# Optimization experiments

Hardware: AMD Instinct MI355X
Metric: run time of the kernel (lower is better)

Reference implementation:

```python
import jax, jax.numpy as jnp
import numpy as np

HIDDEN = 2048
N_HEADS = 32
N_KV_HEADS = 4
HEAD_DIM = 128
EPS = 1e-6
ROPE_THETA = 1000000.0
B, S = 1, 2048


def setup_inputs() -> dict:
    key = jax.random.key(0)
    ks = jax.random.split(key, 7)
    scale = 0.02
    return {
        "hidden_states": jax.random.normal(ks[0], (B, S, HIDDEN), jnp.float32),
        "wq": jax.random.normal(ks[1], (HIDDEN, N_HEADS * HEAD_DIM), jnp.float32) * scale,
        "wk": jax.random.normal(ks[2], (HIDDEN, N_KV_HEADS * HEAD_DIM), jnp.float32) * scale,
        "wv": jax.random.normal(ks[3], (HIDDEN, N_KV_HEADS * HEAD_DIM), jnp.float32) * scale,
        "wo": jax.random.normal(ks[4], (N_HEADS * HEAD_DIM, HIDDEN), jnp.float32) * scale,
        "q_norm_w": jnp.ones((HEAD_DIM,), jnp.float32),
        "k_norm_w": jnp.ones((HEAD_DIM,), jnp.float32),
    }


def _rmsnorm(x, w, eps=EPS):
    # RMSNorm over last (head_dim) axis, as in Qwen3MoeRMSNorm applied per-head
    var = jnp.mean(jnp.square(x), axis=-1, keepdims=True)
    return x * jax.lax.rsqrt(var + eps) * w


def _rope_cos_sin(seq_len, dtype):
    inv_freq = 1.0 / (ROPE_THETA ** (jnp.arange(0, HEAD_DIM, 2, dtype=jnp.float32) / HEAD_DIM))
    pos = jnp.arange(seq_len, dtype=jnp.float32)
    freqs = pos[:, None] * inv_freq[None, :]          # [S, dh/2]
    emb = jnp.concatenate([freqs, freqs], axis=-1)    # [S, dh]
    return jnp.cos(emb).astype(dtype), jnp.sin(emb).astype(dtype)


def _rotate_half(x):
    h = x.shape[-1] // 2
    return jnp.concatenate([-x[..., h:], x[..., :h]], axis=-1)


def reference(hidden_states, wq, wk, wv, wo, q_norm_w, k_norm_w):
    b, s, _ = hidden_states.shape
    # QKV projections (bias-free)
    q = (hidden_states @ wq).reshape(b, s, N_HEADS, HEAD_DIM)
    k = (hidden_states @ wk).reshape(b, s, N_KV_HEADS, HEAD_DIM)
    v = (hidden_states @ wv).reshape(b, s, N_KV_HEADS, HEAD_DIM)
    # per-head RMSNorm on Q and K
    q = _rmsnorm(q, q_norm_w)
    k = _rmsnorm(k, k_norm_w)
    # RoPE (prefill, start_pos = 0)
    cos, sin = _rope_cos_sin(s, q.dtype)              # [S, dh]
    cos = cos[None, :, None, :]
    sin = sin[None, :, None, :]
    q = q * cos + _rotate_half(q) * sin
    k = k * cos + _rotate_half(k) * sin
    # GQA: repeat KV heads to match Q heads
    groups = N_HEADS // N_KV_HEADS
    k = jnp.repeat(k, groups, axis=2)                 # [B,S,nH,dh]
    v = jnp.repeat(v, groups, axis=2)
    # causal SDPA
    scaling = HEAD_DIM ** -0.5
    scores = jnp.einsum("bqhd,bkhd->bhqk", q, k) * scaling
    causal = jnp.tril(jnp.ones((s, s), dtype=bool))
    scores = jnp.where(causal[None, None], scores, jnp.finfo(scores.dtype).min)
    probs = jax.nn.softmax(scores, axis=-1)
    attn = jnp.einsum("bhqk,bkhd->bqhd", probs, v)    # [B,S,nH,dh]
    attn = attn.reshape(b, s, N_HEADS * HEAD_DIM)
    return attn @ wo
```

## Files before the change

kernel.cpp:

```cpp
#include <hip/hip_runtime.h>
#include <stdint.h>

typedef unsigned short u16;
typedef __bf16 bf16x8 __attribute__((ext_vector_type(8)));
typedef float f32x4 __attribute__((ext_vector_type(4)));

#define SEQ 2048
#define QKV_N 5120
#define QN 4096

#if __has_builtin(__builtin_amdgcn_exp2f)
#define EXP2F __builtin_amdgcn_exp2f
#else
#define EXP2F exp2f
#endif

#define QSC (0.08838834764831845f * 1.4426950408889634f)
#define MLOG2E 17.312340490667560f

#define WAIT_VM(n) asm volatile("s_waitcnt vmcnt(" #n ")" ::: "memory")
#define WAIT_LGKM asm volatile("s_waitcnt lgkmcnt(0)" ::: "memory")
#define FENCE asm volatile("" ::: "memory")
#define BARRIER_RAW do { FENCE; __builtin_amdgcn_s_barrier(); FENCE; } while (0)

__device__ __forceinline__ u16 f2bf(float f) {
  union { float f; unsigned u; } v; v.f = f;
  unsigned r = v.u + 0x7fffu + ((v.u >> 16) & 1u);
  return (u16)(r >> 16);
}
__device__ __forceinline__ u16 f2bf_fast(float f) {
  union { float f; unsigned u; } v; v.f = f;
  return (u16)((v.u + 0x8000u) >> 16);
}
__device__ __forceinline__ float bf2f(u16 b) {
  union { unsigned u; float f; } v; v.u = ((unsigned)b) << 16;
  return v.f;
}

__device__ __forceinline__ void gl2lds16(const void* g, void* l) {
  __builtin_amdgcn_global_load_lds((const __attribute__((address_space(1))) void*)g,
                                   (__attribute__((address_space(3))) void*)l, 16, 0, 0);
}

__global__ __launch_bounds__(256) void k_prep(const float* __restrict__ hidden,
                                              const float* __restrict__ wq, const float* __restrict__ wk,
                                              const float* __restrict__ wv, const float* __restrict__ wo,
                                              u16* __restrict__ hid_bf, u16* __restrict__ WT,
                                              u16* __restrict__ woT) {
  __shared__ float t[32][33];
  int bx = blockIdx.x;
  if (bx < 4096) {
    int i = (bx * 256 + threadIdx.x) * 4;
    float4 v = *(const float4*)(hidden + i);
    ushort4 o;
    o.x = f2bf(v.x); o.y = f2bf(v.y); o.z = f2bf(v.z); o.w = f2bf(v.w);
    *(ushort4*)(hid_bf + i) = o;
    return;
  }
  const float* src; u16* dst; int R, C, cx, cy;
  if (bx < 4096 + 8192) {
    int local = bx - 4096; src = wq; dst = WT; R = 2048; C = 4096;
    cx = local & 127; cy = local >> 7;
  } else if (bx < 4096 + 8192 + 1024) {
    int local = bx - (4096 + 8192); src = wk; dst = WT + (size_t)4096 * 2048; R = 2048; C = 512;
    cx = local & 15; cy = local >> 4;
  } else if (bx < 4096 + 8192 + 2048) {
    int local = bx - (4096 + 8192 + 1024); src = wv; dst = WT + (size_t)4608 * 2048; R = 2048; C = 512;
    cx = local & 15; cy = local >> 4;
  } else {
    int local = bx - (4096 + 8192 + 2048); src = wo; dst = woT; R = 4096; C = 2048;
    cx = local & 63; cy = local >> 6;
  }
  int c0 = cx * 32, r0 = cy * 32;
  int j = threadIdx.x & 31, i0 = threadIdx.x >> 5;
#pragma unroll
  for (int p = 0; p < 4; ++p) {
    int r = i0 + p * 8;
    t[r][j] = src[(size_t)(r0 + r) * C + c0 + j];
  }
  __syncthreads();
#pragma unroll
  for (int p = 0; p < 4; ++p) {
    int r = i0 + p * 8;
    dst[(size_t)(c0 + r) * R + r0 + j] = f2bf(t[j][r]);
  }
}

__global__ __launch_bounds__(256) void k_gemm160(const u16* __restrict__ A, const u16* __restrict__ BT,
                                                 u16* __restrict__ C, int M, int N, int K) {
  __shared__ u16 As[2][128 * 64];
  __shared__ u16 Bs[2][160 * 64];
  const int tid = threadIdx.x;
  const int w = tid >> 6, lane = tid & 63, quad = lane >> 4, l15 = lane & 15;
  const int m0 = blockIdx.y * 128, n0 = blockIdx.x * 160;
  const int mw = (w & 1) * 64, nw = (w >> 1) * 80;

  f32x4 acc[4][5];
#pragma unroll
  for (int i = 0; i < 4; ++i)
#pragma unroll
    for (int j = 0; j < 5; ++j) acc[i][j] = {0.f, 0.f, 0.f, 0.f};

  auto stage = [&](int kt, int buf) {
    const int k0 = kt << 6;
#pragma unroll
    for (int p = 0; p < 4; ++p) {
      int ci = (w * 4 + p) * 64 + lane;
      int row = ci >> 3, gc = (ci & 7) ^ (row & 7);
      gl2lds16(A + (size_t)(m0 + row) * K + k0 + gc * 8, &As[buf][(w * 4 + p) * 512]);
    }
#pragma unroll
    for (int p = 0; p < 5; ++p) {
      int ci = (w * 5 + p) * 64 + lane;
      int row = ci >> 3, gc = (ci & 7) ^ (row & 7);
      gl2lds16(BT + (size_t)(n0 + row) * K + k0 + gc * 8, &Bs[buf][(w * 5 + p) * 512]);
    }
  };

  const int nk = K >> 6;
  stage(0, 0);
  for (int kt = 0; kt < nk; ++kt) {
    WAIT_LGKM;
    BARRIER_RAW;
    if (kt + 1 < nk) {
      stage(kt + 1, (kt + 1) & 1);
      WAIT_VM(9);
    } else {
      WAIT_VM(0);
    }
    BARRIER_RAW;
    const u16* Ac = As[kt & 1];
    const u16* Bc = Bs[kt & 1];
#pragma unroll
    for (int kk = 0; kk < 2; ++kk) {
      bf16x8 a[4], b[5];
#pragma unroll
      for (int mt = 0; mt < 4; ++mt) {
        int row = mw + mt * 16 + l15;
        a[mt] = *(const bf16x8*)(Ac + row * 64 + (((kk * 4 + quad) ^ (row & 7)) * 8));
      }
#pragma unroll
      for (int nt = 0; nt < 5; ++nt) {
        int row = nw + nt * 16 + l15;
        b[nt] = *(const bf16x8*)(Bc + row * 64 + (((kk * 4 + quad) ^ (row & 7)) * 8));
      }
#pragma unroll
      for (int mt = 0; mt < 4; ++mt)
#pragma unroll
        for (int nt = 0; nt < 5; ++nt)
          acc[mt][nt] = __builtin_amdgcn_mfma_f32_16x16x32_bf16(a[mt], b[nt], acc[mt][nt], 0, 0, 0);
    }
  }
#pragma unroll
  for (int mt = 0; mt < 4; ++mt)
#pragma unroll
    for (int nt = 0; nt < 5; ++nt)
#pragma unroll
      for (int r = 0; r < 4; ++r) {
        int row = m0 + mw + mt * 16 + quad * 4 + r;
        int col = n0 + nw + nt * 16 + l15;
        C[(size_t)row * N + col] = f2bf(acc[mt][nt][r]);
      }
}

__global__ __launch_bounds__(256) void k_gemm_sk(const u16* __restrict__ A, const u16* __restrict__ BT,
                                                 float* __restrict__ C, int M, int N, int K) {
  __shared__ u16 As[2][128 * 64];
  __shared__ u16 Bs[2][128 * 64];
  const int tid = threadIdx.x;
  const int w = tid >> 6, lane = tid & 63, quad = lane >> 4, l15 = lane & 15;
  const int m0 = blockIdx.y * 128, n0 = blockIdx.x * 128;
  const int mw = (w & 1) * 64, nw = (w >> 1) * 64;
  const int khalf = K >> 1;
  const int kbase = blockIdx.z * khalf;

  f32x4 acc[4][4];
#pragma unroll
  for (int i = 0; i < 4; ++i)
#pragma unroll
    for (int j = 0; j < 4; ++j) acc[i][j] = {0.f, 0.f, 0.f, 0.f};

  auto stage = [&](int kt, int buf) {
    const int k0 = kbase + (kt << 6);
#pragma unroll
    for (int p = 0; p < 4; ++p) {
      int ci = (w * 4 + p) * 64 + lane;
      int row = ci >> 3, gc = (ci & 7) ^ (row & 7);
      gl2lds16(A + (size_t)(m0 + row) * K + k0 + gc * 8, &As[buf][(w * 4 + p) * 512]);
      gl2lds16(BT + (size_t)(n0 + row) * K + k0 + gc * 8, &Bs[buf][(w * 4 + p) * 512]);
    }
  };

  const int nk = khalf >> 6;
  stage(0, 0);
  for (int kt = 0; kt < nk; ++kt) {
    WAIT_LGKM;
    BARRIER_RAW;
    if (kt + 1 < nk) {
      stage(kt + 1, (kt + 1) & 1);
      WAIT_VM(8);
    } else {
      WAIT_VM(0);
    }
    BARRIER_RAW;
    const u16* Ac = As[kt & 1];
    const u16* Bc = Bs[kt & 1];
#pragma unroll
    for (int kk = 0; kk < 2; ++kk) {
      bf16x8 a[4], b[4];
#pragma unroll
      for (int mt = 0; mt < 4; ++mt) {
        int row = mw + mt * 16 + l15;
        a[mt] = *(const bf16x8*)(Ac + row * 64 + (((kk * 4 + quad) ^ (row & 7)) * 8));
      }
#pragma unroll
      for (int nt = 0; nt < 4; ++nt) {
        int row = nw + nt * 16 + l15;
        b[nt] = *(const bf16x8*)(Bc + row * 64 + (((kk * 4 + quad) ^ (row & 7)) * 8));
      }
#pragma unroll
      for (int mt = 0; mt < 4; ++mt)
#pragma unroll
        for (int nt = 0; nt < 4; ++nt)
          acc[mt][nt] = __builtin_amdgcn_mfma_f32_16x16x32_bf16(a[mt], b[nt], acc[mt][nt], 0, 0, 0);
    }
  }
#pragma unroll
  for (int mt = 0; mt < 4; ++mt)
#pragma unroll
    for (int nt = 0; nt < 4; ++nt)
#pragma unroll
      for (int r = 0; r < 4; ++r) {
        int row = m0 + mw + mt * 16 + quad * 4 + r;
        int col = n0 + nw + nt * 16 + l15;
        atomicAdd(&C[(size_t)row * N + col], acc[mt][nt][r]);
      }
}

__global__ __launch_bounds__(256) void k_post(const u16* __restrict__ QKV,
                                              const float* __restrict__ qw, const float* __restrict__ kw,
                                              u16* __restrict__ qb, u16* __restrict__ kb,
                                              u16* __restrict__ vt) {
  __shared__ u16 t[32][34];
  int bx = blockIdx.x;
  if (bx < 2048) {
    int s = bx;
    int w = threadIdx.x >> 6, lane = threadIdx.x & 63;
    const u16* row = QKV + (size_t)s * QKV_N;
    float inv_freq = EXP2F(-(float)lane * (19.931568569324174f / 64.0f));
    float fr = (float)s * inv_freq;
    float sn, cs;
    __sincosf(fr, &sn, &cs);
    float qw0 = qw[lane], qw1 = qw[lane + 64];
    float kw0 = kw[lane], kw1 = kw[lane + 64];
    for (int item = w; item < 36; item += 4) {
      bool isq = item < 32;
      int h = isq ? item : item - 32;
      int base = isq ? h * 128 : 4096 + h * 128;
      float x0 = bf2f(row[base + lane]), x1 = bf2f(row[base + 64 + lane]);
      float ss = x0 * x0 + x1 * x1;
#pragma unroll
      for (int off = 1; off < 64; off <<= 1) ss += __shfl_xor(ss, off);
      float rr = rsqrtf(ss * (1.0f / 128.0f) + 1e-6f);
      float n0 = x0 * rr * (isq ? qw0 : kw0), n1 = x1 * rr * (isq ? qw1 : kw1);
      float y0 = n0 * cs - n1 * sn;
      float y1 = n1 * cs + n0 * sn;
      if (isq) {
        size_t o = (size_t)s * QN + h * 128 + lane;
        qb[o] = f2bf(y0 * QSC);
        qb[o + 64] = f2bf(y1 * QSC);
      } else {
        size_t o = ((size_t)h * SEQ + s) * 128 + lane;
        kb[o] = f2bf(y0);
        kb[o + 64] = f2bf(y1);
      }
    }
    return;
  }
  int local = bx - 2048;
  int s0 = (local & 63) * 32, d0 = ((local >> 6) & 3) * 32, h = local >> 8;
  int j = threadIdx.x & 31, i0 = threadIdx.x >> 5;
#pragma unroll
  for (int p = 0; p < 4; ++p) {
    int r = i0 + p * 8;
    t[r][j] = QKV[(size_t)(s0 + r) * QKV_N + 4608 + h * 128 + d0 + j];
  }
  __syncthreads();
#pragma unroll
  for (int p = 0; p < 4; ++p) {
    int r = i0 + p * 8;
    vt[((size_t)h * 128 + d0 + r) * SEQ + s0 + j] = t[j][r];
  }
}

__global__ __launch_bounds__(256, 2) void k_flash(const u16* __restrict__ qb_, const u16* __restrict__ kb,
                                                  const u16* __restrict__ vt, u16* __restrict__ attn) {
  __shared__ u16 Ks[2][64 * 128];
  __shared__ u16 Vts[2][128 * 64];
  __shared__ u16 Ps[4][2048];
  const int bx = blockIdx.x;
  const int slot = bx & 255, phase = bx >> 8;
  const int head = slot & 31;
  const int qblk = phase ? (slot >> 5) : 15 - (slot >> 5);
  const int kvh = head >> 3;
  const int q0 = qblk * 128;
  const int tid = threadIdx.x, w = tid >> 6, lane = tid & 63, quad = lane >> 4, l15 = lane & 15;
  const int rowlo0 = q0 + w * 32, rowlo1 = rowlo0 + 16;

  bf16x8 qf[2][4];
#pragma unroll
  for (int mt = 0; mt < 2; ++mt) {
    const u16* qrow = qb_ + (size_t)(rowlo0 + mt * 16 + l15) * QN + head * 128;
#pragma unroll
    for (int ks = 0; ks < 4; ++ks) qf[mt][ks] = *(const bf16x8*)(qrow + ks * 32 + quad * 8);
  }
  f32x4 o[2][8];
#pragma unroll
  for (int mt = 0; mt < 2; ++mt)
#pragma unroll
    for (int i = 0; i < 8; ++i) o[mt][i] = {0.f, 0.f, 0.f, 0.f};
  float lr[2][4] = {{0.f, 0.f, 0.f, 0.f}, {0.f, 0.f, 0.f, 0.f}};

  const u16* kbase = kb + (size_t)kvh * SEQ * 128;
  const u16* vbase = vt + (size_t)kvh * 128 * SEQ;
  u16* pw = Ps[w];

  auto stage = [&](int ti, int buf) {
    const int t0 = ti * 64;
#pragma unroll
    for (int p = 0; p < 4; ++p) {
      int ci = (w * 4 + p) * 64 + lane;
      {
        int row = ci >> 4, gc = (ci & 15) ^ (row & 15);
        gl2lds16(kbase + (size_t)(t0 + row) * 128 + gc * 8, &Ks[buf][(w * 4 + p) * 512]);
      }
      {
        int d = ci >> 3, gc = (ci & 7) ^ (d & 7);
        gl2lds16(vbase + (size_t)d * SEQ + t0 + gc * 8, &Vts[buf][(w * 4 + p) * 512]);
      }
    }
  };

  const int nT = 2 * qblk + 2;
  stage(0, 0);
  for (int ti = 0; ti < nT; ++ti) {
    const int t0 = ti * 64;
    WAIT_LGKM;
    BARRIER_RAW;
    if (ti + 1 < nT) {
      stage(ti + 1, (ti + 1) & 1);
      WAIT_VM(8);
    } else {
      WAIT_VM(0);
    }
    BARRIER_RAW;
    const u16* Kc = Ks[ti & 1];
    const u16* Vc = Vts[ti & 1];

    const bool a0 = t0 < rowlo0 + 16;
    const bool a1 = t0 < rowlo1 + 16;
    if (a1) {
      f32x4 sa[2][4];
#pragma unroll
      for (int mt = 0; mt < 2; ++mt)
#pragma unroll
        for (int nt = 0; nt < 4; ++nt) sa[mt][nt] = {0.f, 0.f, 0.f, 0.f};
#pragma unroll
      for (int nt = 0; nt < 4; ++nt) {
        int row = nt * 16 + l15;
#pragma unroll
        for (int ks = 0; ks < 4; ++ks) {
          bf16x8 kf = *(const bf16x8*)(Kc + row * 128 + (((ks * 4 + quad) ^ (row & 15)) * 8));
          if (a0) sa[0][nt] = __builtin_amdgcn_mfma_f32_16x16x32_bf16(qf[0][ks], kf, sa[0][nt], 0, 0, 0);
          sa[1][nt] = __builtin_amdgcn_mfma_f32_16x16x32_bf16(qf[1][ks], kf, sa[1][nt], 0, 0, 0);
        }
      }
#pragma unroll
      for (int mt = 0; mt < 2; ++mt) {
        if (mt == 0 && !a0) continue;
        const int rl = rowlo0 + mt * 16;
        const bool domask = (t0 + 63 > rl);
        u16* pm = pw + mt * 1024;
#pragma unroll
        for (int nt = 0; nt < 4; ++nt)
#pragma unroll
          for (int r = 0; r < 4; ++r) {
            float p = EXP2F(sa[mt][nt][r] - MLOG2E);
            if (domask) {
              int tcol = t0 + nt * 16 + l15;
              int qrow = rl + quad * 4 + r;
              p = (tcol > qrow) ? 0.f : p;
            }
            sa[mt][nt][r] = p;
            pm[(quad * 4 + r) * 64 + ((nt ^ quad) << 4) + l15] = f2bf_fast(p);
          }
#pragma unroll
        for (int r = 0; r < 4; ++r)
          lr[mt][r] += sa[mt][0][r] + sa[mt][1][r] + sa[mt][2][r] + sa[mt][3][r];
      }
      WAIT_LGKM;
#pragma unroll
      for (int ks2 = 0; ks2 < 2; ++ks2) {
        int col = (ks2 * 32 + quad * 8) ^ ((l15 >> 2) << 4);
        bf16x8 pa0, pa1;
        if (a0) pa0 = *(const bf16x8*)(pw + l15 * 64 + col);
        pa1 = *(const bf16x8*)(pw + 1024 + l15 * 64 + col);
#pragma unroll
        for (int nt2 = 0; nt2 < 8; ++nt2) {
          int d = nt2 * 16 + l15;
          bf16x8 vf = *(const bf16x8*)(Vc + d * 64 + (((ks2 * 4 + quad) ^ (d & 7)) * 8));
          if (a0) o[0][nt2] = __builtin_amdgcn_mfma_f32_16x16x32_bf16(pa0, vf, o[0][nt2], 0, 0, 0);
          o[1][nt2] = __builtin_amdgcn_mfma_f32_16x16x32_bf16(pa1, vf, o[1][nt2], 0, 0, 0);
        }
      }
    }
  }
#pragma unroll
  for (int mt = 0; mt < 2; ++mt) {
    float inv[4];
#pragma unroll
    for (int r = 0; r < 4; ++r) {
      float s = lr[mt][r];
      s += __shfl_xor(s, 1);
      s += __shfl_xor(s, 2);
      s += __shfl_xor(s, 4);
      s += __shfl_xor(s, 8);
      inv[r] = 1.0f / s;
    }
#pragma unroll
    for (int nt2 = 0; nt2 < 8; ++nt2)
#pragma unroll
      for (int r = 0; r < 4; ++r) {
        size_t idx = (size_t)(rowlo0 + mt * 16 + quad * 4 + r) * QN + head * 128 + nt2 * 16 + l15;
        attn[idx] = f2bf_fast(o[mt][nt2][r] * inv[r]);
      }
  }
}

extern "C" void kernel_launch(void* const* d_in, const int* in_sizes, int n_in,
                              void* d_out, int out_size, void* d_ws, size_t ws_size,
                              hipStream_t stream) {
  const float* hidden = (const float*)d_in[0];
  const float* wq = (const float*)d_in[1];
  const float* wk = (const float*)d_in[2];
  const float* wv = (const float*)d_in[3];
  const float* wo = (const float*)d_in[4];
  const float* qnw = (const float*)d_in[5];
  const float* knw = (const float*)d_in[6];
  float* out = (float*)d_out;

  char* ws = (char*)d_ws;
  u16* hid_bf = (u16*)(ws);
  u16* WT = (u16*)(ws + 8388608);
  u16* woT = (u16*)(ws + 29360128);
  u16* QKV = (u16*)(ws + 46137344);
  u16* q_bf = (u16*)(ws + 88080384);
  u16* k_bf = (u16*)(ws + 104857600);
  u16* vt = (u16*)(ws + 106954752);
  u16* attn = (u16*)(ws + 109051904);

  hipMemsetAsync(d_out, 0, (size_t)2048 * 2048 * 4, stream);
  k_prep<<<22528, 256, 0, stream>>>(hidden, wq, wk, wv, wo, hid_bf, WT, woT);
  k_gemm160<<<dim3(32, 16), 256, 0, stream>>>(hid_bf, WT, QKV, 2048, 5120, 2048);
  k_post<<<3072, 256, 0, stream>>>(QKV, qnw, knw, q_bf, k_bf, vt);
  k_flash<<<512, 256, 0, stream>>>(q_bf, k_bf, vt, attn);
  k_gemm_sk<<<dim3(16, 16, 2), 256, 0, stream>>>(attn, woT, out, 2048, 2048, 4096);
}
```

Measured before the change: 325.7 us.

## Pair mirrored causal query blocks per workgroup to balance flash attention work

Each workgroup now handles two 64-row query slabs, one early (a) and one mirrored late (31-a), so every block runs a near-equal number of KV tiles. This replaces the earlier scheme of 128-row contiguous query blocks with long-first ordering, which left per-block work uneven. The trade-off is that each wave's two 16-row tiles are far apart, so the early tile sits idle for most KV iterations and its MFMAs are skipped. Grid size and launch code are assumed to stay at 512 blocks.

```diff
diff --git a/kernel.cpp b/kernel.cpp
--- a/kernel.cpp
+++ b/kernel.cpp
@@ -299,18 +299,18 @@
   __shared__ u16 Vts[2][128 * 64];
   __shared__ u16 Ps[4][2048];
   const int bx = blockIdx.x;
-  const int slot = bx & 255, phase = bx >> 8;
-  const int head = slot & 31;
-  const int qblk = phase ? (slot >> 5) : 15 - (slot >> 5);
+  const int head = bx & 31;
+  const int a = bx >> 5;
   const int kvh = head >> 3;
-  const int q0 = qblk * 128;
   const int tid = threadIdx.x, w = tid >> 6, lane = tid & 63, quad = lane >> 4, l15 = lane & 15;
-  const int rowlo0 = q0 + w * 32, rowlo1 = rowlo0 + 16;
+  const int rA = a * 64 + w * 16;
+  const int rB = (31 - a) * 64 + w * 16;
 
   bf16x8 qf[2][4];
 #pragma unroll
   for (int mt = 0; mt < 2; ++mt) {
-    const u16* qrow = qb_ + (size_t)(rowlo0 + mt * 16 + l15) * QN + head * 128;
+    const int rbase = mt ? rB : rA;
+    const u16* qrow = qb_ + (size_t)(rbase + l15) * QN + head * 128;
 #pragma unroll
     for (int ks = 0; ks < 4; ++ks) qf[mt][ks] = *(const bf16x8*)(qrow + ks * 32 + quad * 8);
   }
@@ -341,7 +341,7 @@
     }
   };
 
-  const int nT = 2 * qblk + 2;
+  const int nT = 32 - a;
   stage(0, 0);
   for (int ti = 0; ti < nT; ++ti) {
     const int t0 = ti * 64;
@@ -357,9 +357,8 @@
     const u16* Kc = Ks[ti & 1];
     const u16* Vc = Vts[ti & 1];
 
-    const bool a0 = t0 < rowlo0 + 16;
-    const bool a1 = t0 < rowlo1 + 16;
-    if (a1) {
+    const bool aA = t0 < rA + 16;
+    {
       f32x4 sa[2][4];
 #pragma unroll
       for (int mt = 0; mt < 2; ++mt)
@@ -371,14 +370,14 @@
 #pragma unroll
         for (int ks = 0; ks < 4; ++ks) {
           bf16x8 kf = *(const bf16x8*)(Kc + row * 128 + (((ks * 4 + quad) ^ (row & 15)) * 8));
-          if (a0) sa[0][nt] = __builtin_amdgcn_mfma_f32_16x16x32_bf16(qf[0][ks], kf, sa[0][nt], 0, 0, 0);
+          if (aA) sa[0][nt] = __builtin_amdgcn_mfma_f32_16x16x32_bf16(qf[0][ks], kf, sa[0][nt], 0, 0, 0);
           sa[1][nt] = __builtin_amdgcn_mfma_f32_16x16x32_bf16(qf[1][ks], kf, sa[1][nt], 0, 0, 0);
         }
       }
 #pragma unroll
       for (int mt = 0; mt < 2; ++mt) {
-        if (mt == 0 && !a0) continue;
-        const int rl = rowlo0 + mt * 16;
+        if (mt == 0 && !aA) continue;
+        const int rl = mt ? rB : rA;
         const bool domask = (t0 + 63 > rl);
         u16* pm = pw + mt * 1024;
 #pragma unroll
@@ -403,13 +402,13 @@
       for (int ks2 = 0; ks2 < 2; ++ks2) {
         int col = (ks2 * 32 + quad * 8) ^ ((l15 >> 2) << 4);
         bf16x8 pa0, pa1;
-        if (a0) pa0 = *(const bf16x8*)(pw + l15 * 64 + col);
+        if (aA) pa0 = *(const bf16x8*)(pw + l15 * 64 + col);
         pa1 = *(const bf16x8*)(pw + 1024 + l15 * 64 + col);
 #pragma unroll
         for (int nt2 = 0; nt2 < 8; ++nt2) {
           int d = nt2 * 16 + l15;
           bf16x8 vf = *(const bf16x8*)(Vc + d * 64 + (((ks2 * 4 + quad) ^ (d & 7)) * 8));
-          if (a0) o[0][nt2] = __builtin_amdgcn_mfma_f32_16x16x32_bf16(pa0, vf, o[0][nt2], 0, 0, 0);
+          if (aA) o[0][nt2] = __builtin_amdgcn_mfma_f32_16x16x32_bf16(pa0, vf, o[0][nt2], 0, 0, 0);
           o[1][nt2] = __builtin_amdgcn_mfma_f32_16x16x32_bf16(pa1, vf, o[1][nt2], 0, 0, 0);
         }
       }
@@ -417,6 +416,7 @@
   }
 #pragma unroll
   for (int mt = 0; mt < 2; ++mt) {
+    const int rbase = mt ? rB : rA;
     float inv[4];
 #pragma unroll
     for (int r = 0; r < 4; ++r) {
@@ -431,7 +431,7 @@
     for (int nt2 = 0; nt2 < 8; ++nt2)
 #pragma unroll
       for (int r = 0; r < 4; ++r) {
-        size_t idx = (size_t)(rowlo0 + mt * 16 + quad * 4 + r) * QN + head * 128 + nt2 * 16 + l15;
+        size_t idx = (size_t)(rbase + quad * 4 + r) * QN + head * 128 + nt2 * 16 + l15;
         attn[idx] = f2bf_fast(o[mt][nt2][r] * inv[r]);
       }
   }
```

Result: no change. 323.8 us (-0.6%).
